# Kernel tuning notes

Hardware: AMD Instinct MI355X
Metric: run time of the kernel (lower is better)

Reference implementation:

```python
import jax, jax.numpy as jnp
import numpy as np

EPS = 1e-5

def _ln(x, g, b):
    mu = jnp.mean(x, axis=-1, keepdims=True)
    var = jnp.mean(jnp.square(x - mu), axis=-1, keepdims=True)
    return (x - mu) * jax.lax.rsqrt(var + EPS) * g + b

def setup_inputs() -> dict:
    B, T, D, E, H, M = 2, 2048, 1024, 8, 512, 2048
    key = jax.random.key(0)
    ks = jax.random.split(key, 24)
    s = 0.02
    inp = {}
    inp['x'] = jax.random.normal(ks[0], (B, T, D), jnp.float32)
    flat = jnp.arange(M, dtype=jnp.int32) * 2  # unique token ids over B*T
    inp['index_b'] = flat // T
    inp['index_t'] = flat % T
    # shared SwiGLU (hidden = H)
    inp['sw1'] = jax.random.normal(ks[1], (H, D), jnp.float32) * s
    inp['sb1'] = jnp.zeros((H,), jnp.float32)
    inp['sw2'] = jax.random.normal(ks[2], (H, D), jnp.float32) * s
    inp['sb2'] = jnp.zeros((H,), jnp.float32)
    inp['sw3'] = jax.random.normal(ks[3], (D, H), jnp.float32) * s
    inp['sb3'] = jnp.zeros((D,), jnp.float32)
    inp['s_ln_g'] = jnp.ones((H,), jnp.float32)
    inp['s_ln_b'] = jnp.zeros((H,), jnp.float32)
    # gates
    inp['sg_w'] = jax.random.normal(ks[4], (1, D), jnp.float32) * s
    inp['sg_b'] = jnp.zeros((1,), jnp.float32)
    inp['eg_w'] = jax.random.normal(ks[5], (E, D), jnp.float32) * s
    inp['eg_b'] = jnp.zeros((E,), jnp.float32)
    inp['exp_bias'] = jnp.zeros((E,), jnp.float32)
    # per-expert SwiGLU stacks
    inp['ew1'] = jax.random.normal(ks[6], (E, H, D), jnp.float32) * s
    inp['eb1'] = jnp.zeros((E, H), jnp.float32)
    inp['ew2'] = jax.random.normal(ks[7], (E, H, D), jnp.float32) * s
    inp['eb2'] = jnp.zeros((E, H), jnp.float32)
    inp['ew3'] = jax.random.normal(ks[8], (E, D, H), jnp.float32) * s
    inp['eb3'] = jnp.zeros((E, D), jnp.float32)
    inp['sel_ln_g'] = jnp.ones((H,), jnp.float32)
    inp['sel_ln_b'] = jnp.zeros((H,), jnp.float32)
    return inp

def _forward(x, index_b, index_t, sw1, sb1, sw2, sb2, sw3, sb3, s_ln_g, s_ln_b,
             sg_w, sg_b, eg_w, eg_b, exp_bias, ew1, eb1, ew2, eb2, ew3, eb3,
             sel_ln_g, sel_ln_b):
    # shared SwiGLU over all tokens: [B,T,D]
    x1 = jnp.einsum('btd,hd->bth', x, sw1) + sb1
    x2 = jnp.einsum('btd,hd->bth', x, sw2) + sb2
    sh = _ln(jax.nn.silu(x1) * x2, s_ln_g, s_ln_b)
    shared_out = jnp.einsum('bth,dh->btd', sh, sw3) + sb3
    # MoE tokens
    x_moe = x[index_b, index_t]  # [M,D]
    shared_scores = jax.nn.sigmoid(x_moe @ sg_w.T + sg_b)       # [M,1]
    expert_scores = jax.nn.sigmoid(x_moe @ eg_w.T + eg_b)       # [M,E]
    top1_idx = jnp.argmax(expert_scores + exp_bias, axis=-1)    # [M]
    top1_score = jnp.take_along_axis(expert_scores, top1_idx[:, None], axis=-1)  # [M,1]
    weights = jax.nn.softmax(jnp.concatenate([shared_scores, top1_score], axis=-1), axis=-1)
    shared_w, expert_w = weights[:, 0], weights[:, 1]
    shared_moe_out = shared_out[index_b, index_t] * shared_w[:, None]
    # per-expert SwiGLU computed densely for all E, then token selects its expert
    h1 = jnp.einsum('md,ehd->meh', x_moe, ew1) + eb1  # [M,E,H]
    h2 = jnp.einsum('md,ehd->meh', x_moe, ew2) + eb2
    z = _ln(jax.nn.silu(h1) * h2, sel_ln_g, sel_ln_b)
    out_all = jnp.einsum('meh,edh->med', z, ew3) + eb3  # [M,E,D]
    expert_out = jnp.take_along_axis(out_all, top1_idx[:, None, None], axis=1)[:, 0]  # [M,D]
    expert_moe_out = expert_out * expert_w[:, None]
    final_out = shared_out.at[index_b, index_t].set(shared_moe_out + expert_moe_out)
    return final_out

def reference(x, index_b, index_t, sw1, sb1, sw2, sb2, sw3, sb3, s_ln_g, s_ln_b,
              sg_w, sg_b, eg_w, eg_b, exp_bias, ew1, eb1, ew2, eb2, ew3, eb3,
              sel_ln_g, sel_ln_b):
    return _forward(x, index_b, index_t, sw1, sb1, sw2, sb2, sw3, sb3, s_ln_g, s_ln_b,
                    sg_w, sg_b, eg_w, eg_b, exp_bias, ew1, eb1, ew2, eb2, ew3, eb3,
                    sel_ln_g, sel_ln_b)
```

## Files before the change

### kernel.cpp

```cpp
#include <hip/hip_runtime.h>
#include <cstdint>

typedef unsigned short u16;
typedef __bf16 bf16x8 __attribute__((ext_vector_type(8)));
typedef float f32x4 __attribute__((ext_vector_type(4)));

#define T_SEQ  2048
#define D_DIM  1024
#define H_DIM  512
#define E_NUM  8
#define M_TOK  2048
#define BT_TOK 4096
#define MAXP   3072
#define NSPLIT_NONE (1 << 28)

static __device__ __forceinline__ u16 f2bf(float f) {
    union { float f; uint32_t u; } v; v.f = f;
    uint32_t u = v.u;
    return (u16)((u + 0x7FFFu + ((u >> 16) & 1u)) >> 16);
}
static __device__ __forceinline__ uint32_t pack2(float a, float b) {
    return (uint32_t)f2bf(a) | ((uint32_t)f2bf(b) << 16);
}

static __device__ __forceinline__ void gl_lds16(const u16* g, u16* l) {
    __builtin_amdgcn_global_load_lds(
        (const __attribute__((address_space(1))) uint32_t*)g,
        (__attribute__((address_space(3))) uint32_t*)l, 16, 0, 0);
}


__device__ __forceinline__ void gating_body(
    int m,
    const float* __restrict__ x,
    const int* __restrict__ ib, const int* __restrict__ itx,
    const float* __restrict__ sgw, const float* __restrict__ sgb,
    const float* __restrict__ egw, const float* __restrict__ egb,
    const float* __restrict__ ebias,
    float* __restrict__ shw, float* __restrict__ expw,
    int* __restrict__ top1, int* __restrict__ rowidx,
    float* xs, float* sc)
{
    int tid = threadIdx.x;
    int row = ib[m] * T_SEQ + itx[m];
    if (tid == 0) rowidx[m] = row;
    const float* xr = x + (size_t)row * D_DIM;
    ((float4*)xs)[tid] = ((const float4*)xr)[tid];
    __syncthreads();
    int lane = tid & 63, w = tid >> 6;
    for (int sidx = w; sidx < 9; sidx += 4) {
        const float* wr = (sidx == 0) ? sgw : (egw + (size_t)(sidx - 1) * D_DIM);
        float acc = 0.f;
        for (int i = lane; i < D_DIM; i += 64) acc += xs[i] * wr[i];
        #pragma unroll
        for (int o = 32; o > 0; o >>= 1) acc += __shfl_xor(acc, o);
        if (lane == 0) sc[sidx] = acc;
    }
    __syncthreads();
    if (tid == 0) {
        float ss = 1.f / (1.f + expf(-(sc[0] + sgb[0])));
        float es[E_NUM];
        float best = -1e30f; int bi = 0;
        #pragma unroll
        for (int e = 0; e < E_NUM; ++e) {
            es[e] = 1.f / (1.f + expf(-(sc[1 + e] + egb[e])));
            float t = es[e] + ebias[e];
            if (t > best) { best = t; bi = e; }
        }
        float ts = es[bi];
        shw[m]  = 1.f / (1.f + expf(ts - ss));
        expw[m] = 1.f / (1.f + expf(ss - ts));
        top1[m] = bi;
    }
}

__device__ __forceinline__ void bucket_body(
    const int* __restrict__ top1,
    int* __restrict__ base, int* __restrict__ cnt, int* __restrict__ perm,
    int* sm)
{
    int* lc  = sm;
    int* lb  = sm + E_NUM;
    int* cur = sm + 2 * E_NUM + 1;
    int tid = threadIdx.x;
    if (tid < E_NUM) { lc[tid] = 0; cur[tid] = 0; }
    __syncthreads();
    for (int m = tid; m < M_TOK; m += 256) atomicAdd(&lc[top1[m]], 1);
    __syncthreads();
    if (tid == 0) {
        int bacc = 0;
        for (int e = 0; e < E_NUM; ++e) { lb[e] = bacc; bacc += (lc[e] + 63) & ~63; }
        lb[E_NUM] = bacc;
    }
    __syncthreads();
    for (int m = tid; m < M_TOK; m += 256) {
        int e = top1[m];
        int pos = lb[e] + atomicAdd(&cur[e], 1);
        perm[pos] = m;
    }
    if (tid <= E_NUM) base[tid] = lb[tid];
    if (tid < E_NUM)  cnt[tid]  = lc[tid];
}

template<bool SEL>
__device__ __forceinline__ void ln_body(
    int m,
    const float* __restrict__ X,
    const float* __restrict__ g, const float* __restrict__ b,
    u16* __restrict__ out,
    const int* __restrict__ base, const int* __restrict__ cnt,
    float* red)
{
    int tid = threadIdx.x;
    if (SEL) {
        bool valid = false;
        int tot = base[E_NUM];
        if (m < tot) {
            int e = 0;
            while (!(m >= base[e] && m < base[e + 1])) ++e;
            valid = (m - base[e]) < cnt[e];
        }
        if (!valid) {
            out[(size_t)m * H_DIM + tid] = 0;
            out[(size_t)m * H_DIM + tid + 256] = 0;
            return;
        }
    }
    const float* row = X + (size_t)m * D_DIM;
    float a0 = row[tid],       c0 = row[H_DIM + tid];
    float a1 = row[tid + 256], c1 = row[H_DIM + tid + 256];
    float v0 = (a0 / (1.f + expf(-a0))) * c0;
    float v1 = (a1 / (1.f + expf(-a1))) * c1;
    float s = v0 + v1, s2 = v0 * v0 + v1 * v1;
    #pragma unroll
    for (int o = 32; o > 0; o >>= 1) {
        s  += __shfl_xor(s, o);
        s2 += __shfl_xor(s2, o);
    }
    int w = tid >> 6;
    if ((tid & 63) == 0) { red[w] = s; red[4 + w] = s2; }
    __syncthreads();
    s  = red[0] + red[1] + red[2] + red[3];
    s2 = red[4] + red[5] + red[6] + red[7];
    float mu  = s * (1.f / H_DIM);
    float var = s2 * (1.f / H_DIM) - mu * mu;
    float inv = rsqrtf(var + 1e-5f);
    out[(size_t)m * H_DIM + tid]       = f2bf((v0 - mu) * inv * g[tid] + b[tid]);
    out[(size_t)m * H_DIM + tid + 256] = f2bf((v1 - mu) * inv * g[tid + 256] + b[tid + 256]);
}

template<int MODE, int KLEN>
__device__ __forceinline__ void gemm_body(
    int bn, int bm,
    const u16* __restrict__ A, int lda,
    const u16* __restrict__ W0, const u16* __restrict__ W1, int nsplit,
    const float* __restrict__ b0, const float* __restrict__ b1,
    float* __restrict__ C,
    const int* __restrict__ base, const int* __restrict__ cnt,
    const int* __restrict__ perm, const int* __restrict__ rowidx,
    const float* __restrict__ shw, const float* __restrict__ expw,
    u16* lds)
{
    constexpr int NITER = KLEN / 64;
    const int tid   = threadIdx.x;
    const int mbase = bm * 64;

    int pend = 0;
    if (MODE >= 2) {
        const int tot = base[E_NUM];
        if (mbase >= tot) return;
        int e = 0;
        while (!(mbase >= base[e] && mbase < base[e + 1])) ++e;
        pend = base[e] + cnt[e];
        if (mbase >= pend) return;
        const size_t wstride = (size_t)H_DIM * D_DIM;
        W0 += (size_t)e * wstride;
        if (MODE == 2) W1 += (size_t)e * wstride;
        b0 += e * ((MODE == 2) ? H_DIM : D_DIM);
        if (MODE == 2) b1 += e * H_DIM;
    }

    const int w  = tid >> 6;
    const int l  = tid & 63;
    const int sr = tid >> 3;
    const int sc = tid & 7;

    const u16* agp[2];
    #pragma unroll
    for (int t = 0; t < 2; ++t) {
        int r = t * 32 + sr;
        int grow;
        if (MODE == 2) {
            int p  = mbase + r;
            int pp = (p < pend) ? p : (pend - 1);
            grow = rowidx[perm[pp]];
        } else {
            grow = mbase + r;
        }
        agp[t] = A + (size_t)grow * lda + (sc ^ (r & 7)) * 8;
    }
    const u16* bgp[4];
    #pragma unroll
    for (int t = 0; t < 4; ++t) {
        int r = t * 32 + sr;
        int n = bn * 128 + r;
        bgp[t] = ((n < nsplit) ? (W0 + (size_t)n * KLEN)
                               : (W1 + (size_t)(n - nsplit) * KLEN)) + (sc ^ (r & 7)) * 8;
    }

    const int l16 = l & 15, quad = l >> 4;
    const int wm = w >> 1, wn = w & 1;

    int avo[2][2], bvo[4][2];
    #pragma unroll
    for (int i = 0; i < 2; ++i) {
        int R = wm * 32 + i * 16 + l16;
        #pragma unroll
        for (int kx = 0; kx < 2; ++kx)
            avo[i][kx] = R * 128 + (((kx * 4 + quad) ^ (R & 7)) * 16);
    }
    #pragma unroll
    for (int j = 0; j < 4; ++j) {
        int R = wn * 64 + j * 16 + l16;
        #pragma unroll
        for (int kx = 0; kx < 2; ++kx)
            bvo[j][kx] = 8192 + R * 128 + (((kx * 4 + quad) ^ (R & 7)) * 16);
    }

    f32x4 acc[2][4];
    #pragma unroll
    for (int i = 0; i < 2; ++i)
        #pragma unroll
        for (int j = 0; j < 4; ++j)
            acc[i][j] = (f32x4){0.f, 0.f, 0.f, 0.f};

    const int kstart = (bm + bn * 3) & (NITER - 1);
    const char* ldsc = (const char*)lds;

    {
        int k0 = (kstart & (NITER - 1)) * 64;
        #pragma unroll
        for (int t = 0; t < 2; ++t)
            gl_lds16(agp[t] + k0, lds + t * 2048 + w * 512);
        #pragma unroll
        for (int t = 0; t < 4; ++t)
            gl_lds16(bgp[t] + k0, lds + 4096 + t * 2048 + w * 512);
    }
    __syncthreads();

    for (int it = 0; it < NITER; ++it) {
        const int cur = it & 1;
        if (it + 1 < NITER) {
            int k0 = ((it + 1 + kstart) & (NITER - 1)) * 64;
            u16* lb = lds + (cur ^ 1) * 12288;
            #pragma unroll
            for (int t = 0; t < 2; ++t)
                gl_lds16(agp[t] + k0, lb + t * 2048 + w * 512);
            #pragma unroll
            for (int t = 0; t < 4; ++t)
                gl_lds16(bgp[t] + k0, lb + 4096 + t * 2048 + w * 512);
        }
        const char* lb = ldsc + cur * 24576;
        #pragma unroll
        for (int kx = 0; kx < 2; ++kx) {
            bf16x8 av[2], bv[4];
            #pragma unroll
            for (int i = 0; i < 2; ++i)
                av[i] = *(const bf16x8*)(lb + avo[i][kx]);
            #pragma unroll
            for (int j = 0; j < 4; ++j)
                bv[j] = *(const bf16x8*)(lb + bvo[j][kx]);
            #pragma unroll
            for (int i = 0; i < 2; ++i)
                #pragma unroll
                for (int j = 0; j < 4; ++j)
                    acc[i][j] = __builtin_amdgcn_mfma_f32_16x16x32_bf16(av[i], bv[j], acc[i][j], 0, 0, 0);
        }
        if (it + 1 < NITER) __syncthreads();
    }

    if (MODE == 3) {
        #pragma unroll
        for (int i = 0; i < 2; ++i) {
            #pragma unroll
            for (int rr = 0; rr < 4; ++rr) {
                int p = mbase + wm * 32 + i * 16 + quad * 4 + rr;
                if (p < pend) {
                    int tok = perm[p];
                    int row = rowidx[tok];
                    float sw = shw[tok], ew = expw[tok];
                    float* outr = C + (size_t)row * D_DIM;
                    #pragma unroll
                    for (int j = 0; j < 4; ++j) {
                        int gn = bn * 128 + wn * 64 + j * 16 + l16;
                        outr[gn] = outr[gn] * sw + (acc[i][j][rr] + b0[gn]) * ew;
                    }
                }
            }
        }
    } else {
        #pragma unroll
        for (int i = 0; i < 2; ++i) {
            #pragma unroll
            for (int rr = 0; rr < 4; ++rr) {
                int gm = mbase + wm * 32 + i * 16 + quad * 4 + rr;
                float* outr = C + (size_t)gm * D_DIM;
                #pragma unroll
                for (int j = 0; j < 4; ++j) {
                    int gn = bn * 128 + wn * 64 + j * 16 + l16;
                    float bias = (gn < nsplit) ? b0[gn] : b1[gn - nsplit];
                    outr[gn] = acc[i][j][rr] + bias;
                }
            }
        }
    }
}


__global__ __launch_bounds__(256)
void k_cvt_gating(const float* __restrict__ x,
                  const float* __restrict__ sw1, const float* __restrict__ sw2,
                  const float* __restrict__ sw3,
                  const float* __restrict__ ew1, const float* __restrict__ ew2,
                  const float* __restrict__ ew3,
                  u16* __restrict__ xb,
                  u16* __restrict__ sw1b, u16* __restrict__ sw2b, u16* __restrict__ sw3b,
                  u16* __restrict__ ew1b, u16* __restrict__ ew2b, u16* __restrict__ ew3b,
                  const int* __restrict__ ib, const int* __restrict__ itx,
                  const float* __restrict__ sgw, const float* __restrict__ sgb,
                  const float* __restrict__ egw, const float* __restrict__ egb,
                  const float* __restrict__ ebias,
                  float* __restrict__ shw, float* __restrict__ expw,
                  int* __restrict__ top1, int* __restrict__ rowidx)
{
    __shared__ __align__(16) float smem[D_DIM + 16];
    int bx = blockIdx.x;
    if (bx < M_TOK) {
        gating_body(bx, x, ib, itx, sgw, sgb, egw, egb, ebias,
                    shw, expw, top1, rowidx, smem, smem + D_DIM);
        return;
    }
    long i = (long)(bx - M_TOK) * 256 + threadIdx.x;
    const float* s; u16* d; long off;
    if      (i < 1048576) { s = x;   d = xb;   off = i; }
    else if (i < 1179648) { s = sw1; d = sw1b; off = i - 1048576; }
    else if (i < 1310720) { s = sw2; d = sw2b; off = i - 1179648; }
    else if (i < 1441792) { s = sw3; d = sw3b; off = i - 1310720; }
    else if (i < 2490368) { s = ew1; d = ew1b; off = i - 1441792; }
    else if (i < 3538944) { s = ew2; d = ew2b; off = i - 2490368; }
    else                  { s = ew3; d = ew3b; off = i - 3538944; }
    float4 v = ((const float4*)s)[off];
    uint2 o;
    o.x = pack2(v.x, v.y);
    o.y = pack2(v.z, v.w);
    ((uint2*)d)[off] = o;
}

__global__ __launch_bounds__(256, 4)
void k_g1_bucket(const u16* __restrict__ xb,
                 const u16* __restrict__ sw1b, const u16* __restrict__ sw2b,
                 const float* __restrict__ sb1, const float* __restrict__ sb2,
                 float* __restrict__ x12,
                 const int* __restrict__ top1,
                 int* __restrict__ basep, int* __restrict__ cntp, int* __restrict__ perm)
{
    __shared__ __align__(16) u16 lds[2 * (64 + 128) * 64];
    int bx = blockIdx.x;
    if (bx < 512) {
        gemm_body<0, 1024>(bx & 7, bx >> 3, xb, D_DIM, sw1b, sw2b, H_DIM, sb1, sb2, x12,
                           nullptr, nullptr, nullptr, nullptr, nullptr, nullptr, lds);
    } else {
        bucket_body(top1, basep, cntp, perm, (int*)lds);
    }
}

__global__ __launch_bounds__(256)
void k_ln(const float* __restrict__ x12,
          const float* __restrict__ g, const float* __restrict__ b,
          u16* __restrict__ shn)
{
    __shared__ __align__(16) float smf[8];
    ln_body<false>(blockIdx.x, x12, g, b, shn, nullptr, nullptr, smf);
}

__global__ __launch_bounds__(256, 4)
void k_g2_e1(const u16* __restrict__ shn, const u16* __restrict__ sw3b,
             const float* __restrict__ sb3, float* __restrict__ out,
             const u16* __restrict__ xb,
             const u16* __restrict__ ew1b, const u16* __restrict__ ew2b,
             const float* __restrict__ eb1, const float* __restrict__ eb2,
             float* __restrict__ h12,
             const int* __restrict__ basep, const int* __restrict__ cntp,
             const int* __restrict__ perm, const int* __restrict__ rowidx)
{
    __shared__ __align__(16) u16 lds[2 * (64 + 128) * 64];
    int bx = blockIdx.x;
    if (bx < 512) {
        gemm_body<1, 512>(bx & 7, bx >> 3, shn, H_DIM, sw3b, sw3b, NSPLIT_NONE, sb3, sb3, out,
                          nullptr, nullptr, nullptr, nullptr, nullptr, nullptr, lds);
    } else {
        int b2 = bx - 512;
        gemm_body<2, 1024>(b2 & 7, b2 >> 3, xb, D_DIM, ew1b, ew2b, H_DIM, eb1, eb2, h12,
                           basep, cntp, perm, rowidx, nullptr, nullptr, lds);
    }
}

__global__ __launch_bounds__(256)
void k_ln_sel(const float* __restrict__ h12,
              const float* __restrict__ g, const float* __restrict__ b,
              u16* __restrict__ z,
              const int* __restrict__ basep, const int* __restrict__ cntp)
{
    __shared__ __align__(16) float smf[8];
    ln_body<true>(blockIdx.x, h12, g, b, z, basep, cntp, smf);
}

__global__ __launch_bounds__(256, 4)
void k_e2(const u16* __restrict__ z, const u16* __restrict__ ew3b,
          const float* __restrict__ eb3, float* __restrict__ out,
          const int* __restrict__ basep, const int* __restrict__ cntp,
          const int* __restrict__ perm, const int* __restrict__ rowidx,
          const float* __restrict__ shw, const float* __restrict__ expw)
{
    __shared__ __align__(16) u16 lds[2 * (64 + 128) * 64];
    int bx = blockIdx.x;
    gemm_body<3, 512>(bx & 7, bx >> 3, z, H_DIM, ew3b, ew3b, NSPLIT_NONE, eb3, eb3, out,
                      basep, cntp, perm, rowidx, shw, expw, lds);
}

extern "C" void kernel_launch(void* const* d_in, const int* in_sizes, int n_in,
                              void* d_out, int out_size, void* d_ws, size_t ws_size,
                              hipStream_t stream) {
    const float* x        = (const float*)d_in[0];
    const int*   index_b  = (const int*)d_in[1];
    const int*   index_t  = (const int*)d_in[2];
    const float* sw1      = (const float*)d_in[3];
    const float* sb1      = (const float*)d_in[4];
    const float* sw2      = (const float*)d_in[5];
    const float* sb2      = (const float*)d_in[6];
    const float* sw3      = (const float*)d_in[7];
    const float* sb3      = (const float*)d_in[8];
    const float* s_ln_g   = (const float*)d_in[9];
    const float* s_ln_b   = (const float*)d_in[10];
    const float* sg_w     = (const float*)d_in[11];
    const float* sg_b     = (const float*)d_in[12];
    const float* eg_w     = (const float*)d_in[13];
    const float* eg_b     = (const float*)d_in[14];
    const float* exp_bias = (const float*)d_in[15];
    const float* ew1      = (const float*)d_in[16];
    const float* eb1      = (const float*)d_in[17];
    const float* ew2      = (const float*)d_in[18];
    const float* eb2      = (const float*)d_in[19];
    const float* ew3      = (const float*)d_in[20];
    const float* eb3      = (const float*)d_in[21];
    const float* sel_ln_g = (const float*)d_in[22];
    const float* sel_ln_b = (const float*)d_in[23];
    float* out = (float*)d_out;
    char*  ws  = (char*)d_ws;

    u16*   xb   = (u16*)(ws + 0);
    u16*   sw1b = (u16*)(ws + 8388608);
    u16*   sw2b = (u16*)(ws + 9437184);
    u16*   sw3b = (u16*)(ws + 10485760);
    u16*   ew1b = (u16*)(ws + 11534336);
    u16*   ew2b = (u16*)(ws + 19922944);
    u16*   ew3b = (u16*)(ws + 28311552);
    float* x12  = (float*)(ws + 36700160);
    float* h12  = x12;
    u16*   sh   = (u16*)(ws + 53477376);
    u16*   z    = sh;
    float* shw    = (float*)(ws + 57671680);
    float* expw   = shw + M_TOK;
    int*   top1   = (int*)(expw + M_TOK);
    int*   rowidx = top1 + M_TOK;
    int*   perm   = rowidx + M_TOK;
    int*   basep  = perm + MAXP;
    int*   cntp   = basep + 16;

    k_cvt_gating<<<dim3(M_TOK + 17920), dim3(256), 0, stream>>>(
        x, sw1, sw2, sw3, ew1, ew2, ew3,
        xb, sw1b, sw2b, sw3b, ew1b, ew2b, ew3b,
        index_b, index_t, sg_w, sg_b, eg_w, eg_b, exp_bias,
        shw, expw, top1, rowidx);

    k_g1_bucket<<<dim3(512 + 1), dim3(256), 0, stream>>>(
        xb, sw1b, sw2b, sb1, sb2, x12, top1, basep, cntp, perm);

    k_ln<<<dim3(BT_TOK), dim3(256), 0, stream>>>(x12, s_ln_g, s_ln_b, sh);

    k_g2_e1<<<dim3(512 + 8 * (MAXP / 64)), dim3(256), 0, stream>>>(
        sh, sw3b, sb3, out,
        xb, ew1b, ew2b, eb1, eb2, h12,
        basep, cntp, perm, rowidx);

    k_ln_sel<<<dim3(MAXP), dim3(256), 0, stream>>>(
        h12, sel_ln_g, sel_ln_b, z, basep, cntp);

    k_e2<<<dim3(8 * (MAXP / 64)), dim3(256), 0, stream>>>(
        z, ew3b, eb3, out, basep, cntp, perm, rowidx, shw, expw);
}
```

Baseline: 231.9 us.

## Enlarge GEMM tiles to 128x128 and drop LDS double buffering

The GEMM tile grows from 64x128 to 128x128 rows per block, and expert buckets are padded to 128. The double-buffered LDS prefetch becomes a single buffer with a sync before and after each k-step, and the launch bounds no longer request 4 blocks per CU. The gating dot product is vectorised with float4, the expert lookup loop is replaced by an unrolled compare, and gating blocks move to the end of the conversion grid. Bigger tiles raise operand reuse and halve the block count. In exchange the kernel loses load/compute overlap, uses more registers so occupancy may drop, and wastes more padding on small expert buckets.

```diff
diff --git a/kernel.cpp b/kernel.cpp
--- a/kernel.cpp
+++ b/kernel.cpp
@@ -27,6 +27,14 @@
     __builtin_amdgcn_global_load_lds(
         (const __attribute__((address_space(1))) uint32_t*)g,
         (__attribute__((address_space(3))) uint32_t*)l, 16, 0, 0);
+}
+
+static __device__ __forceinline__ int find_expert(int m, const int* __restrict__ base) {
+    int e = 0;
+    #pragma unroll
+    for (int ee = 0; ee < E_NUM - 1; ++ee)
+        if (m >= base[ee + 1]) e = ee + 1;
+    return e;
 }
 
 
@@ -47,11 +55,17 @@
     const float* xr = x + (size_t)row * D_DIM;
     ((float4*)xs)[tid] = ((const float4*)xr)[tid];
     __syncthreads();
-    int lane = tid & 63, w = tid >> 6;
-    for (int sidx = w; sidx < 9; sidx += 4) {
+    int lane = tid & 63, w4 = tid >> 6;
+    for (int sidx = w4; sidx < 9; sidx += 4) {
         const float* wr = (sidx == 0) ? sgw : (egw + (size_t)(sidx - 1) * D_DIM);
         float acc = 0.f;
-        for (int i = lane; i < D_DIM; i += 64) acc += xs[i] * wr[i];
+        #pragma unroll
+        for (int i = 0; i < 4; ++i) {
+            int idx = i * 64 + lane;
+            float4 xv = ((const float4*)xs)[idx];
+            float4 wv = ((const float4*)wr)[idx];
+            acc += xv.x * wv.x + xv.y * wv.y + xv.z * wv.z + xv.w * wv.w;
+        }
         #pragma unroll
         for (int o = 32; o > 0; o >>= 1) acc += __shfl_xor(acc, o);
         if (lane == 0) sc[sidx] = acc;
@@ -89,7 +103,7 @@
     __syncthreads();
     if (tid == 0) {
         int bacc = 0;
-        for (int e = 0; e < E_NUM; ++e) { lb[e] = bacc; bacc += (lc[e] + 63) & ~63; }
+        for (int e = 0; e < E_NUM; ++e) { lb[e] = bacc; bacc += (lc[e] + 127) & ~127; }
         lb[E_NUM] = bacc;
     }
     __syncthreads();
@@ -116,8 +130,7 @@
         bool valid = false;
         int tot = base[E_NUM];
         if (m < tot) {
-            int e = 0;
-            while (!(m >= base[e] && m < base[e + 1])) ++e;
+            int e = find_expert(m, base);
             valid = (m - base[e]) < cnt[e];
         }
         if (!valid) {
@@ -163,14 +176,13 @@
 {
     constexpr int NITER = KLEN / 64;
     const int tid   = threadIdx.x;
-    const int mbase = bm * 64;
+    const int mbase = bm * 128;
 
     int pend = 0;
     if (MODE >= 2) {
         const int tot = base[E_NUM];
         if (mbase >= tot) return;
-        int e = 0;
-        while (!(mbase >= base[e] && mbase < base[e + 1])) ++e;
+        int e = find_expert(mbase, base);
         pend = base[e] + cnt[e];
         if (mbase >= pend) return;
         const size_t wstride = (size_t)H_DIM * D_DIM;
@@ -185,9 +197,9 @@
     const int sr = tid >> 3;
     const int sc = tid & 7;
 
-    const u16* agp[2];
-    #pragma unroll
-    for (int t = 0; t < 2; ++t) {
+    const u16* agp[4];
+    #pragma unroll
+    for (int t = 0; t < 4; ++t) {
         int r = t * 32 + sr;
         int grow;
         if (MODE == 2) {
@@ -211,25 +223,21 @@
     const int l16 = l & 15, quad = l >> 4;
     const int wm = w >> 1, wn = w & 1;
 
-    int avo[2][2], bvo[4][2];
-    #pragma unroll
-    for (int i = 0; i < 2; ++i) {
-        int R = wm * 32 + i * 16 + l16;
-        #pragma unroll
-        for (int kx = 0; kx < 2; ++kx)
-            avo[i][kx] = R * 128 + (((kx * 4 + quad) ^ (R & 7)) * 16);
+    int avo[4], bvo[4];
+    #pragma unroll
+    for (int i = 0; i < 4; ++i) {
+        int R = wm * 64 + i * 16 + l16;
+        avo[i] = R * 128 + ((quad ^ (R & 7)) * 16);
     }
     #pragma unroll
     for (int j = 0; j < 4; ++j) {
         int R = wn * 64 + j * 16 + l16;
-        #pragma unroll
-        for (int kx = 0; kx < 2; ++kx)
-            bvo[j][kx] = 8192 + R * 128 + (((kx * 4 + quad) ^ (R & 7)) * 16);
-    }
-
-    f32x4 acc[2][4];
-    #pragma unroll
-    for (int i = 0; i < 2; ++i)
+        bvo[j] = 16384 + R * 128 + ((quad ^ (R & 7)) * 16);
+    }
+
+    f32x4 acc[4][4];
+    #pragma unroll
+    for (int i = 0; i < 4; ++i)
         #pragma unroll
         for (int j = 0; j < 4; ++j)
             acc[i][j] = (f32x4){0.f, 0.f, 0.f, 0.f};
@@ -237,54 +245,39 @@
     const int kstart = (bm + bn * 3) & (NITER - 1);
     const char* ldsc = (const char*)lds;
 
-    {
-        int k0 = (kstart & (NITER - 1)) * 64;
-        #pragma unroll
-        for (int t = 0; t < 2; ++t)
+    for (int it = 0; it < NITER; ++it) {
+        int k0 = ((it + kstart) & (NITER - 1)) * 64;
+        #pragma unroll
+        for (int t = 0; t < 4; ++t)
             gl_lds16(agp[t] + k0, lds + t * 2048 + w * 512);
         #pragma unroll
         for (int t = 0; t < 4; ++t)
-            gl_lds16(bgp[t] + k0, lds + 4096 + t * 2048 + w * 512);
-    }
-    __syncthreads();
-
-    for (int it = 0; it < NITER; ++it) {
-        const int cur = it & 1;
-        if (it + 1 < NITER) {
-            int k0 = ((it + 1 + kstart) & (NITER - 1)) * 64;
-            u16* lb = lds + (cur ^ 1) * 12288;
+            gl_lds16(bgp[t] + k0, lds + 8192 + t * 2048 + w * 512);
+        __syncthreads();
+        #pragma unroll
+        for (int kx = 0; kx < 2; ++kx) {
+            bf16x8 av[4], bv[4];
             #pragma unroll
-            for (int t = 0; t < 2; ++t)
-                gl_lds16(agp[t] + k0, lb + t * 2048 + w * 512);
-            #pragma unroll
-            for (int t = 0; t < 4; ++t)
-                gl_lds16(bgp[t] + k0, lb + 4096 + t * 2048 + w * 512);
-        }
-        const char* lb = ldsc + cur * 24576;
-        #pragma unroll
-        for (int kx = 0; kx < 2; ++kx) {
-            bf16x8 av[2], bv[4];
-            #pragma unroll
-            for (int i = 0; i < 2; ++i)
-                av[i] = *(const bf16x8*)(lb + avo[i][kx]);
+            for (int i = 0; i < 4; ++i)
+                av[i] = *(const bf16x8*)(ldsc + (avo[i] ^ (kx * 64)));
             #pragma unroll
             for (int j = 0; j < 4; ++j)
-                bv[j] = *(const bf16x8*)(lb + bvo[j][kx]);
+                bv[j] = *(const bf16x8*)(ldsc + (bvo[j] ^ (kx * 64)));
             #pragma unroll
-            for (int i = 0; i < 2; ++i)
+            for (int i = 0; i < 4; ++i)
                 #pragma unroll
                 for (int j = 0; j < 4; ++j)
                     acc[i][j] = __builtin_amdgcn_mfma_f32_16x16x32_bf16(av[i], bv[j], acc[i][j], 0, 0, 0);
         }
-        if (it + 1 < NITER) __syncthreads();
+        __syncthreads();
     }
 
     if (MODE == 3) {
         #pragma unroll
-        for (int i = 0; i < 2; ++i) {
+        for (int i = 0; i < 4; ++i) {
             #pragma unroll
             for (int rr = 0; rr < 4; ++rr) {
-                int p = mbase + wm * 32 + i * 16 + quad * 4 + rr;
+                int p = mbase + wm * 64 + i * 16 + quad * 4 + rr;
                 if (p < pend) {
                     int tok = perm[p];
                     int row = rowidx[tok];
@@ -300,10 +293,10 @@
         }
     } else {
         #pragma unroll
-        for (int i = 0; i < 2; ++i) {
+        for (int i = 0; i < 4; ++i) {
             #pragma unroll
             for (int rr = 0; rr < 4; ++rr) {
-                int gm = mbase + wm * 32 + i * 16 + quad * 4 + rr;
+                int gm = mbase + wm * 64 + i * 16 + quad * 4 + rr;
                 float* outr = C + (size_t)gm * D_DIM;
                 #pragma unroll
                 for (int j = 0; j < 4; ++j) {
@@ -335,12 +328,12 @@
 {
     __shared__ __align__(16) float smem[D_DIM + 16];
     int bx = blockIdx.x;
-    if (bx < M_TOK) {
-        gating_body(bx, x, ib, itx, sgw, sgb, egw, egb, ebias,
+    if (bx >= 17920) {
+        gating_body(bx - 17920, x, ib, itx, sgw, sgb, egw, egb, ebias,
                     shw, expw, top1, rowidx, smem, smem + D_DIM);
         return;
     }
-    long i = (long)(bx - M_TOK) * 256 + threadIdx.x;
+    long i = (long)bx * 256 + threadIdx.x;
     const float* s; u16* d; long off;
     if      (i < 1048576) { s = x;   d = xb;   off = i; }
     else if (i < 1179648) { s = sw1; d = sw1b; off = i - 1048576; }
@@ -356,7 +349,7 @@
     ((uint2*)d)[off] = o;
 }
 
-__global__ __launch_bounds__(256, 4)
+__global__ __launch_bounds__(256)
 void k_g1_bucket(const u16* __restrict__ xb,
                  const u16* __restrict__ sw1b, const u16* __restrict__ sw2b,
                  const float* __restrict__ sb1, const float* __restrict__ sb2,
@@ -364,9 +357,9 @@
                  const int* __restrict__ top1,
                  int* __restrict__ basep, int* __restrict__ cntp, int* __restrict__ perm)
 {
-    __shared__ __align__(16) u16 lds[2 * (64 + 128) * 64];
+    __shared__ __align__(16) u16 lds[(128 + 128) * 64];
     int bx = blockIdx.x;
-    if (bx < 512) {
+    if (bx < 256) {
         gemm_body<0, 1024>(bx & 7, bx >> 3, xb, D_DIM, sw1b, sw2b, H_DIM, sb1, sb2, x12,
                            nullptr, nullptr, nullptr, nullptr, nullptr, nullptr, lds);
     } else {
@@ -383,7 +376,7 @@
     ln_body<false>(blockIdx.x, x12, g, b, shn, nullptr, nullptr, smf);
 }
 
-__global__ __launch_bounds__(256, 4)
+__global__ __launch_bounds__(256)
 void k_g2_e1(const u16* __restrict__ shn, const u16* __restrict__ sw3b,
              const float* __restrict__ sb3, float* __restrict__ out,
              const u16* __restrict__ xb,
@@ -393,13 +386,13 @@
              const int* __restrict__ basep, const int* __restrict__ cntp,
              const int* __restrict__ perm, const int* __restrict__ rowidx)
 {
-    __shared__ __align__(16) u16 lds[2 * (64 + 128) * 64];
+    __shared__ __align__(16) u16 lds[(128 + 128) * 64];
     int bx = blockIdx.x;
-    if (bx < 512) {
+    if (bx < 256) {
         gemm_body<1, 512>(bx & 7, bx >> 3, shn, H_DIM, sw3b, sw3b, NSPLIT_NONE, sb3, sb3, out,
                           nullptr, nullptr, nullptr, nullptr, nullptr, nullptr, lds);
     } else {
-        int b2 = bx - 512;
+        int b2 = bx - 256;
         gemm_body<2, 1024>(b2 & 7, b2 >> 3, xb, D_DIM, ew1b, ew2b, H_DIM, eb1, eb2, h12,
                            basep, cntp, perm, rowidx, nullptr, nullptr, lds);
     }
@@ -415,14 +408,14 @@
     ln_body<true>(blockIdx.x, h12, g, b, z, basep, cntp, smf);
 }
 
-__global__ __launch_bounds__(256, 4)
+__global__ __launch_bounds__(256)
 void k_e2(const u16* __restrict__ z, const u16* __restrict__ ew3b,
           const float* __restrict__ eb3, float* __restrict__ out,
           const int* __restrict__ basep, const int* __restrict__ cntp,
           const int* __restrict__ perm, const int* __restrict__ rowidx,
           const float* __restrict__ shw, const float* __restrict__ expw)
 {
-    __shared__ __align__(16) u16 lds[2 * (64 + 128) * 64];
+    __shared__ __align__(16) u16 lds[(128 + 128) * 64];
     int bx = blockIdx.x;
     gemm_body<3, 512>(bx & 7, bx >> 3, z, H_DIM, ew3b, ew3b, NSPLIT_NONE, eb3, eb3, out,
                       basep, cntp, perm, rowidx, shw, expw, lds);
@@ -477,18 +470,18 @@
     int*   basep  = perm + MAXP;
     int*   cntp   = basep + 16;
 
-    k_cvt_gating<<<dim3(M_TOK + 17920), dim3(256), 0, stream>>>(
+    k_cvt_gating<<<dim3(17920 + M_TOK), dim3(256), 0, stream>>>(
         x, sw1, sw2, sw3, ew1, ew2, ew3,
         xb, sw1b, sw2b, sw3b, ew1b, ew2b, ew3b,
         index_b, index_t, sg_w, sg_b, eg_w, eg_b, exp_bias,
         shw, expw, top1, rowidx);
 
-    k_g1_bucket<<<dim3(512 + 1), dim3(256), 0, stream>>>(
+    k_g1_bucket<<<dim3(256 + 1), dim3(256), 0, stream>>>(
         xb, sw1b, sw2b, sb1, sb2, x12, top1, basep, cntp, perm);
 
     k_ln<<<dim3(BT_TOK), dim3(256), 0, stream>>>(x12, s_ln_g, s_ln_b, sh);
 
-    k_g2_e1<<<dim3(512 + 8 * (MAXP / 64)), dim3(256), 0, stream>>>(
+    k_g2_e1<<<dim3(256 + 8 * (MAXP / 128)), dim3(256), 0, stream>>>(
         sh, sw3b, sb3, out,
         xb, ew1b, ew2b, eb1, eb2, h12,
         basep, cntp, perm, rowidx);
@@ -496,6 +489,6 @@
     k_ln_sel<<<dim3(MAXP), dim3(256), 0, stream>>>(
         h12, sel_ln_g, sel_ln_b, z, basep, cntp);
 
-    k_e2<<<dim3(8 * (MAXP / 64)), dim3(256), 0, stream>>>(
+    k_e2<<<dim3(8 * (MAXP / 128)), dim3(256), 0, stream>>>(
         z, ew3b, eb3, out, basep, cntp, perm, rowidx, shw, expw);
 }
```

New measurement: 247.2 us. 6.6% more time.
